# Kernel tuning notes

Measured on AMD Instinct MI355X. Metric: run time of the kernel, lower is better.

## Reference

```python
import jax, jax.numpy as jnp
import numpy as np

B, N, M = 2, 256, 256  # batch items, bboxes per item, feature dim (output_channel)
BLOCKS = 2             # graph_conv_block_num


def _conv2d(x, w, b):
    # x: [C,H,W], w: [O,I,kh,kw] -> [O,H,W], SAME padding, stride 1
    y = jax.lax.conv_general_dilated(x[None], w, (1, 1), 'SAME',
                                     dimension_numbers=('NCHW', 'OIHW', 'NCHW'))
    return y[0] + b[:, None, None]


def setup_inputs() -> dict:
    key = jax.random.key(0)
    ks = jax.random.split(key, 8)
    s = 0.02  # small init to keep activations tame through conv stack
    return {
        'edge_feats': jax.random.normal(ks[0], (B, N, N, 7), jnp.float32),
        'node_feats': jax.random.normal(ks[1], (B, N, M), jnp.float32),
        'adapter_w': jax.random.normal(ks[2], (M, 7, 1, 1), jnp.float32) * s,
        'adapter_b': jnp.zeros((M,), jnp.float32),
        'conv0_w': jax.random.normal(ks[3], (M, 3 * M, 3, 3), jnp.float32) * s,
        'conv0_b': jnp.zeros((M,), jnp.float32),
        'conv1_w': jax.random.normal(ks[4], (M, M, 3, 3), jnp.float32) * s,
        'conv1_b': jnp.zeros((M,), jnp.float32),
        'last_w': jax.random.normal(ks[5], (M, M, 3, 3), jnp.float32) * s,
        'last_b': jnp.zeros((M,), jnp.float32),
        'att_w': jax.random.normal(ks[6], (1, M, 1, 1), jnp.float32) * s,
        'att_b': jnp.zeros((1,), jnp.float32),
    }


def reference(edge_feats, node_feats, adapter_w, adapter_b, conv0_w, conv0_b,
              conv1_w, conv1_b, last_w, last_b, att_w, att_b):
    def one(e, n):
        # e: [N,N,7], n: [N,M]
        edge = _conv2d(jnp.transpose(e, (2, 0, 1)), adapter_w, adapter_b)  # [M,N,N]
        node = n
        for _ in range(BLOCKS):  # conv weights shared across blocks, as in torch
            nT = node.T  # [M,N]
            # channel layout at (i,j): [node_i | edge_ij | node_j]
            feat = jnp.concatenate([
                jnp.broadcast_to(nT[:, :, None], (M, N, N)),
                edge,
                jnp.broadcast_to(nT[:, None, :], (M, N, N)),
            ], axis=0)  # [3M,N,N]
            feat = jax.nn.relu(_conv2d(feat, conv0_w, conv0_b))
            feat = jax.nn.relu(_conv2d(feat, conv1_w, conv1_b))
            # edge attention: 1x1 conv -> leaky_relu -> softmax over j -> weighted sum
            att = jax.nn.leaky_relu(_conv2d(feat, att_w, att_b))   # [1,N,N]
            coeff = jax.nn.softmax(att, axis=-1)                   # softmax over last dim
            node = jnp.sum(coeff * feat, axis=-1).T                # [N,M]
            edge = jax.nn.relu(_conv2d(feat, last_w, last_b))      # [M,N,N]
        return node, jnp.transpose(edge, (1, 2, 0))  # [N,M], [N,N,M]
    return jax.vmap(one)(edge_feats, node_feats)
```

## Files before the change

kernel.cpp:

```cpp
#include <hip/hip_runtime.h>
#include <hip/hip_bf16.h>

typedef __hip_bfloat16 bf16;
typedef __attribute__((ext_vector_type(8))) short s16x8;
typedef __attribute__((ext_vector_type(4))) float f32x4;

__device__ __forceinline__ float b2f(bf16 x) { return __bfloat162float(x); }
__device__ __forceinline__ bf16 f2b(float x) { return __float2bfloat16(x); }

__device__ __forceinline__ void gld16(const void* g, void* l) {
  __builtin_amdgcn_global_load_lds((const __attribute__((address_space(1))) unsigned int*)g,
                                   (__attribute__((address_space(3))) unsigned int*)l,
                                   16, 0, 0);
}

__global__ __launch_bounds__(256) void fill_sentinel(float* out, int n) {
  int idx = blockIdx.x * 256 + threadIdx.x;
  if (idx < n) out[idx] = 100.0f;
}

__global__ __launch_bounds__(64) void zero_zb(bf16* zb) {
  zb[threadIdx.x * 2] = f2b(0.f);
  zb[threadIdx.x * 2 + 1] = f2b(0.f);
}

__global__ __launch_bounds__(256) void pack_w(const float* __restrict__ c0w,
                                              const float* __restrict__ c1w,
                                              const float* __restrict__ lw,
                                              bf16* wp0, bf16* wp1, bf16* wp2, bf16* wnp) {
  const int SEG = 9 * 256 * 256;
  int idx = blockIdx.x * 256 + threadIdx.x;
  if (idx < 3 * SEG) {
    int which = idx / SEG, r = idx % SEG;
    int s = r >> 16, o = (r >> 8) & 255, c = r & 255;
    int ky = s / 3, kx = s - 3 * ky;
    if (which == 0)      wp0[r] = f2b(c0w[(((size_t)o * 768 + 256 + c) * 3 + ky) * 3 + kx]);
    else if (which == 1) wp1[r] = f2b(c1w[(((size_t)o * 256 + c) * 3 + ky) * 3 + kx]);
    else                 wp2[r] = f2b(lw [(((size_t)o * 256 + c) * 3 + ky) * 3 + kx]);
  } else {
    int r = idx - 3 * SEG;
    int m = r & 255, c = (r >> 8) & 255, tt = r >> 16;
    int ot = tt % 3, t2 = (tt / 3) % 3, p = tt / 9;
    int ky, kx, cin;
    if (p == 0) { kx = t2; ky = ot; cin = c; }
    else        { ky = t2; kx = ot; cin = 512 + c; }
    wnp[r] = f2b(c0w[(((size_t)m * 768 + cin) * 3 + ky) * 3 + kx]);
  }
}

__global__ __launch_bounds__(256) void adapter_k(const float* __restrict__ e,
                                                 const float* __restrict__ aw,
                                                 const float* __restrict__ ab,
                                                 bf16* __restrict__ E) {
  int i = blockIdx.x;
  int m = threadIdx.x;
  __shared__ float se[256 * 7];
  const size_t rb = (size_t)i * (256 * 7);
  for (int idx = m; idx < 256 * 7; idx += 256) se[idx] = e[rb + idx];
  __syncthreads();
  float w[7];
#pragma unroll
  for (int c = 0; c < 7; ++c) w[c] = aw[m * 7 + c];
  float bias = ab[m];
  bf16* ob = E + (size_t)i * 65536 + m;
  for (int j = 0; j < 256; ++j) {
    const float* ej = se + j * 7;
    float a = bias;
#pragma unroll
    for (int c = 0; c < 7; ++c) a += w[c] * ej[c];
    ob[(size_t)j * 256] = f2b(a);
  }
}

template <typename T>
__global__ __launch_bounds__(256) void node_terms(const T* __restrict__ nd,
                                                  const bf16* __restrict__ wnp,
                                                  float* __restrict__ TT) {
  int bid = blockIdx.x;
  int chunk = bid & 63;
  int t = (bid >> 6) % 3;
  int p = bid / 192;
  int tid = threadIdx.x;
  __shared__ float snd[6][256];
  int pos0 = chunk * 4;
  for (int idx = tid; idx < 6 * 256; idx += 256) {
    int r = idx >> 8, c = idx & 255;
    int gp = pos0 - 1 + r;
    snd[r][c] = (gp >= 0 && gp < 256) ? (float)nd[(size_t)gp * 256 + c] : 0.f;
  }
  __syncthreads();
  float acc[4] = {0.f, 0.f, 0.f, 0.f};
  const bf16* wb = wnp + (size_t)((p * 3 + t) * 3) * 65536 + tid;
  for (int c = 0; c < 256; ++c) {
    float w0 = b2f(wb[(size_t)c * 256]);
    float w1 = b2f(wb[(size_t)(65536 + c * 256)]);
    float w2 = b2f(wb[(size_t)(2 * 65536 + c * 256)]);
#pragma unroll
    for (int ii = 0; ii < 4; ++ii)
      acc[ii] += w0 * snd[ii][c] + w1 * snd[ii + 1][c] + w2 * snd[ii + 2][c];
  }
  float* o = TT + (((size_t)(p * 3 + t) * 256 + pos0) * 256) + tid;
#pragma unroll
  for (int ii = 0; ii < 4; ++ii) o[(size_t)ii * 256] = acc[ii];
}

template <int EPI, int F32OUT>
__global__ __launch_bounds__(256, 4)
void conv3x3_k(const bf16* __restrict__ inb, const bf16* __restrict__ wpack,
               const float* __restrict__ bias, void* __restrict__ outv,
               const float* __restrict__ TT, const bf16* __restrict__ zbuf) {
  __shared__ __align__(16) char lB[16384];
  __shared__ __align__(16) char lA[16384];
  const int bid = blockIdx.x;
  const int xcd = bid & 7, slot = bid >> 3;
  const int i = (xcd << 5) + (slot >> 2);
  const int ob = slot & 1, jb = (slot >> 1) & 1;
  const int tid = threadIdx.x;
  const int lane = tid & 63, wid = tid >> 6;
  const int wr = wid >> 1, wc = wid & 1;
  const int lo = lane & 15, hi = lane >> 4;

  f32x4 acc[4][4];
  const f32x4 z = {0.f, 0.f, 0.f, 0.f};
#pragma unroll
  for (int mi = 0; mi < 4; ++mi)
#pragma unroll
    for (int ni = 0; ni < 4; ++ni) acc[mi][ni] = z;

  const int xS = tid >> 3;
  const int Gs = tid & 7;
  for (int s = 0; s < 9; ++s) {
    const int ky = s / 3, kx = s - 3 * ky;
    const int r = i + ky - 1;
    if (r < 0 || r > 255) continue;
    const size_t rowbase = (size_t)r * 65536;
    const int colbase = jb * 128 + kx - 1;
    const size_t wbase = ((size_t)s * 256 + ob * 128) * 256;
    for (int cc = 0; cc < 4; ++cc) {
      __syncthreads();
      const int cb = cc * 64;
#pragma unroll
      for (int ch = 0; ch < 4; ++ch) {
        const int x = ch * 32 + xS;
        const int c = colbase + x;
        const int sw = (Gs ^ (x & 7)) << 3;
        const int ldst = (ch * 256 + wid * 64) << 4;
        const bf16* srcB = (c >= 0 && c <= 255)
            ? inb + rowbase + ((size_t)c << 8) + cb + sw
            : zbuf + sw;
        gld16(srcB, lB + ldst);
        gld16(wpack + wbase + ((size_t)x << 8) + cb + sw, lA + ldst);
      }
      __syncthreads();
#pragma unroll
      for (int kk = 0; kk < 2; ++kk) {
        s16x8 af[4], bfr[4];
        const int g0 = kk * 4 + hi;
        const int gx = (g0 ^ (lo & 7)) << 4;
#pragma unroll
        for (int mi = 0; mi < 4; ++mi) {
          const int x = wr * 64 + mi * 16 + lo;
          af[mi] = *(const s16x8*)(lB + x * 128 + gx);
        }
#pragma unroll
        for (int ni = 0; ni < 4; ++ni) {
          const int x = wc * 64 + ni * 16 + lo;
          bfr[ni] = *(const s16x8*)(lA + x * 128 + gx);
        }
#pragma unroll
        for (int mi = 0; mi < 4; ++mi)
#pragma unroll
          for (int ni = 0; ni < 4; ++ni)
            acc[mi][ni] = __builtin_amdgcn_mfma_f32_16x16x32_bf16(af[mi], bfr[ni], acc[mi][ni], 0, 0, 0);
      }
    }
  }

  const int o_base = ob * 128 + wc * 64 + lo;
  const int j_base = jb * 128 + wr * 64 + hi * 4;
  bf16* orow = (bf16*)outv + (size_t)i * 65536;
  float* orowf = (float*)outv + (size_t)i * 65536;
#pragma unroll
  for (int ni = 0; ni < 4; ++ni) {
    const int o = o_base + ni * 16;
    const float bs = bias[o];
    float ni0 = 0.f, ni1 = 0.f, ni2 = 0.f;
    if (EPI) {
      const float* TI = TT + (size_t)i * 256 + o;
      ni0 = TI[0]; ni1 = TI[65536]; ni2 = TI[2 * 65536];
    }
#pragma unroll
    for (int mi = 0; mi < 4; ++mi) {
#pragma unroll
      for (int r = 0; r < 4; ++r) {
        const int j = j_base + mi * 16 + r;
        float v = acc[mi][ni][r] + bs;
        if (EPI) {
          v += ni1 + (j > 0 ? ni0 : 0.f) + (j < 255 ? ni2 : 0.f);
          const float* TJ = TT + (size_t)3 * 65536 + (size_t)j * 256 + o;
          float nj0 = TJ[0], nj1 = TJ[65536], nj2 = TJ[2 * 65536];
          v += nj1 + (i > 0 ? nj0 : 0.f) + (i < 255 ? nj2 : 0.f);
        }
        v = fmaxf(v, 0.f);
        if (F32OUT) orowf[(size_t)j * 256 + o] = v;
        else        orow[(size_t)j * 256 + o] = f2b(v);
      }
    }
  }
}

template <int F32OUT>
__global__ __launch_bounds__(256) void att_wsum(const bf16* __restrict__ feat,
                                                const float* __restrict__ aw,
                                                const float* __restrict__ ab,
                                                bf16* __restrict__ ndb,
                                                float* __restrict__ ndf) {
  int i = blockIdx.x;
  int tid = threadIdx.x, lane = tid & 63, w = tid >> 6;
  __shared__ float s_aw[256];
  __shared__ float s_att[256];
  __shared__ float s_red[8];
  s_aw[tid] = aw[tid];
  __syncthreads();
  float a0 = s_aw[lane * 4], a1 = s_aw[lane * 4 + 1];
  float a2 = s_aw[lane * 4 + 2], a3 = s_aw[lane * 4 + 3];
  const bf16* fb = feat + (size_t)i * 65536;
  float abv = ab[0];
  for (int jj = 0; jj < 64; ++jj) {
    int j = w * 64 + jj;
    const bf16* f = fb + (size_t)j * 256 + lane * 4;
    float v = a0 * b2f(f[0]) + a1 * b2f(f[1]) + a2 * b2f(f[2]) + a3 * b2f(f[3]);
#pragma unroll
    for (int mk = 32; mk; mk >>= 1) v += __shfl_xor(v, mk);
    if (lane == 0) { float a = v + abv; s_att[j] = a > 0.f ? a : 0.01f * a; }
  }
  __syncthreads();
  float x = s_att[tid];
  float mx = x;
#pragma unroll
  for (int mk = 32; mk; mk >>= 1) mx = fmaxf(mx, __shfl_xor(mx, mk));
  if (lane == 0) s_red[w] = mx;
  __syncthreads();
  mx = fmaxf(fmaxf(s_red[0], s_red[1]), fmaxf(s_red[2], s_red[3]));
  float e = expf(x - mx);
  float sm = e;
#pragma unroll
  for (int mk = 32; mk; mk >>= 1) sm += __shfl_xor(sm, mk);
  if (lane == 0) s_red[4 + w] = sm;
  __syncthreads();
  sm = s_red[4] + s_red[5] + s_red[6] + s_red[7];
  __syncthreads();
  s_att[tid] = e / sm;
  __syncthreads();
  float acc = 0.f;
  for (int j = 0; j < 256; ++j) acc += s_att[j] * b2f(fb[(size_t)j * 256 + tid]);
  if (F32OUT) ndf[(size_t)i * 256 + tid] = acc;
  else        ndb[(size_t)i * 256 + tid] = f2b(acc);
}

extern "C" void kernel_launch(void* const* d_in, const int* in_sizes, int n_in,
                              void* d_out, int out_size, void* d_ws, size_t ws_size,
                              hipStream_t stream) {
  const float* edge_feats = (const float*)d_in[0];
  const float* node_feats = (const float*)d_in[1];
  const float* adapter_w  = (const float*)d_in[2];
  const float* adapter_b  = (const float*)d_in[3];
  const float* conv0_w    = (const float*)d_in[4];
  const float* conv0_b    = (const float*)d_in[5];
  const float* conv1_w    = (const float*)d_in[6];
  const float* conv1_b    = (const float*)d_in[7];
  const float* last_w     = (const float*)d_in[8];
  const float* last_b     = (const float*)d_in[9];
  const float* att_w      = (const float*)d_in[10];
  const float* att_b      = (const float*)d_in[11];
  float* out = (float*)d_out;

  char* ws = (char*)d_ws;
  size_t off = 0;
  bf16* Q   = (bf16*)(ws + off); off += (size_t)256 * 256 * 256 * 2;
  bf16* WP0 = (bf16*)(ws + off); off += (size_t)9 * 65536 * 2;
  bf16* WP1 = (bf16*)(ws + off); off += (size_t)9 * 65536 * 2;
  bf16* WP2 = (bf16*)(ws + off); off += (size_t)9 * 65536 * 2;
  bf16* WNP = (bf16*)(ws + off); off += (size_t)18 * 65536 * 2;
  float* TT = (float*)(ws + off); off += (size_t)2 * 3 * 65536 * 4;
  bf16* ND  = (bf16*)(ws + off); off += (size_t)65536 * 2;
  bf16* ZB  = (bf16*)(ws + off); off += 256;
  if (ws_size < off) {
    fill_sentinel<<<(out_size + 255) / 256, 256, 0, stream>>>(out, out_size);
    return;
  }

  zero_zb<<<1, 64, 0, stream>>>(ZB);
  pack_w<<<11520, 256, 0, stream>>>(conv0_w, conv1_w, last_w, WP0, WP1, WP2, WNP);

  for (int b = 0; b < 2; ++b) {
    bf16* P = (bf16*)(out + 131072 + (size_t)b * 16777216);
    float* edge_out = out + 131072 + (size_t)b * 16777216;
    float* node_out = out + (size_t)b * 65536;
    const float* eb = edge_feats + (size_t)b * 458752;
    const float* nb = node_feats + (size_t)b * 65536;

    adapter_k<<<256, 256, 0, stream>>>(eb, adapter_w, adapter_b, P);
    node_terms<float><<<384, 256, 0, stream>>>(nb, WNP, TT);
    conv3x3_k<1, 0><<<1024, 256, 0, stream>>>(P, WP0, conv0_b, Q, TT, ZB);
    conv3x3_k<0, 0><<<1024, 256, 0, stream>>>(Q, WP1, conv1_b, P, nullptr, ZB);
    att_wsum<0><<<256, 256, 0, stream>>>(P, att_w, att_b, ND, nullptr);
    conv3x3_k<0, 0><<<1024, 256, 0, stream>>>(P, WP2, last_b, Q, nullptr, ZB);
    node_terms<bf16><<<384, 256, 0, stream>>>(ND, WNP, TT);
    conv3x3_k<1, 0><<<1024, 256, 0, stream>>>(Q, WP0, conv0_b, P, TT, ZB);
    conv3x3_k<0, 0><<<1024, 256, 0, stream>>>(P, WP1, conv1_b, Q, nullptr, ZB);
    att_wsum<1><<<256, 256, 0, stream>>>(Q, att_w, att_b, nullptr, node_out);
    conv3x3_k<0, 1><<<1024, 256, 0, stream>>>(Q, WP2, last_b, edge_out, nullptr, ZB);
  }
}
```

Before: 1.256 ms.

## Double-buffer LDS loads in conv3x3 kernel to overlap global loads with MFMA

```diff
diff --git a/kernel.cpp b/kernel.cpp
--- a/kernel.cpp
+++ b/kernel.cpp
@@ -105,12 +105,11 @@
 }
 
 template <int EPI, int F32OUT>
-__global__ __launch_bounds__(256, 4)
+__global__ __launch_bounds__(256, 2)
 void conv3x3_k(const bf16* __restrict__ inb, const bf16* __restrict__ wpack,
                const float* __restrict__ bias, void* __restrict__ outv,
                const float* __restrict__ TT, const bf16* __restrict__ zbuf) {
-  __shared__ __align__(16) char lB[16384];
-  __shared__ __align__(16) char lA[16384];
+  __shared__ __align__(16) char lds[65536];
   const int bid = blockIdx.x;
   const int xcd = bid & 7, slot = bid >> 3;
   const int i = (xcd << 5) + (slot >> 2);
@@ -129,51 +128,74 @@
 
   const int xS = tid >> 3;
   const int Gs = tid & 7;
-  for (int s = 0; s < 9; ++s) {
+
+  const int s_lo = (i == 0) ? 3 : 0;
+  const int s_hi = (i == 255) ? 5 : 8;
+  const int nt = (s_hi - s_lo + 1) * 4;
+
+  auto STAGE = [&](int t, int buf) {
+    const int s = s_lo + (t >> 2);
     const int ky = s / 3, kx = s - 3 * ky;
-    const int r = i + ky - 1;
-    if (r < 0 || r > 255) continue;
-    const size_t rowbase = (size_t)r * 65536;
+    const size_t rowbase = (size_t)(i + ky - 1) * 65536;
     const int colbase = jb * 128 + kx - 1;
     const size_t wbase = ((size_t)s * 256 + ob * 128) * 256;
-    for (int cc = 0; cc < 4; ++cc) {
-      __syncthreads();
-      const int cb = cc * 64;
-#pragma unroll
-      for (int ch = 0; ch < 4; ++ch) {
-        const int x = ch * 32 + xS;
-        const int c = colbase + x;
-        const int sw = (Gs ^ (x & 7)) << 3;
-        const int ldst = (ch * 256 + wid * 64) << 4;
-        const bf16* srcB = (c >= 0 && c <= 255)
-            ? inb + rowbase + ((size_t)c << 8) + cb + sw
-            : zbuf + sw;
-        gld16(srcB, lB + ldst);
-        gld16(wpack + wbase + ((size_t)x << 8) + cb + sw, lA + ldst);
+    const int cb = (t & 3) * 64;
+    char* lBb = lds + buf * 32768;
+    char* lAb = lBb + 16384;
+#pragma unroll
+    for (int ch = 0; ch < 4; ++ch) {
+      const int x = ch * 32 + xS;
+      const int c = colbase + x;
+      const int sw = (Gs ^ (x & 7)) << 3;
+      const int ldst = (ch * 256 + wid * 64) << 4;
+      const bf16* srcB = (c >= 0 && c <= 255)
+          ? inb + rowbase + ((size_t)c << 8) + cb + sw
+          : zbuf + sw;
+      gld16(srcB, lBb + ldst);
+      gld16(wpack + wbase + ((size_t)x << 8) + cb + sw, lAb + ldst);
+    }
+  };
+
+  auto COMPUTE = [&](int buf) {
+    const char* lBb = lds + buf * 32768;
+    const char* lAb = lBb + 16384;
+#pragma unroll
+    for (int kk = 0; kk < 2; ++kk) {
+      s16x8 af[4], bfr[4];
+      const int g0 = kk * 4 + hi;
+      const int gx = (g0 ^ (lo & 7)) << 4;
+#pragma unroll
+      for (int mi = 0; mi < 4; ++mi) {
+        const int x = wr * 64 + mi * 16 + lo;
+        af[mi] = *(const s16x8*)(lBb + x * 128 + gx);
       }
-      __syncthreads();
-#pragma unroll
-      for (int kk = 0; kk < 2; ++kk) {
-        s16x8 af[4], bfr[4];
-        const int g0 = kk * 4 + hi;
-        const int gx = (g0 ^ (lo & 7)) << 4;
-#pragma unroll
-        for (int mi = 0; mi < 4; ++mi) {
-          const int x = wr * 64 + mi * 16 + lo;
-          af[mi] = *(const s16x8*)(lB + x * 128 + gx);
-        }
-#pragma unroll
-        for (int ni = 0; ni < 4; ++ni) {
-          const int x = wc * 64 + ni * 16 + lo;
-          bfr[ni] = *(const s16x8*)(lA + x * 128 + gx);
-        }
-#pragma unroll
-        for (int mi = 0; mi < 4; ++mi)
-#pragma unroll
-          for (int ni = 0; ni < 4; ++ni)
-            acc[mi][ni] = __builtin_amdgcn_mfma_f32_16x16x32_bf16(af[mi], bfr[ni], acc[mi][ni], 0, 0, 0);
+#pragma unroll
+      for (int ni = 0; ni < 4; ++ni) {
+        const int x = wc * 64 + ni * 16 + lo;
+        bfr[ni] = *(const s16x8*)(lAb + x * 128 + gx);
       }
-    }
+#pragma unroll
+      for (int mi = 0; mi < 4; ++mi)
+#pragma unroll
+        for (int ni = 0; ni < 4; ++ni)
+          acc[mi][ni] = __builtin_amdgcn_mfma_f32_16x16x32_bf16(af[mi], bfr[ni], acc[mi][ni], 0, 0, 0);
+    }
+  };
+
+  STAGE(0, 0);
+  for (int t = 0; t < nt; ++t) {
+    const int buf = t & 1;
+    if (t + 1 < nt) {
+      STAGE(t + 1, buf ^ 1);
+      asm volatile("s_waitcnt vmcnt(8)" ::: "memory");
+    } else {
+      asm volatile("s_waitcnt vmcnt(0)" ::: "memory");
+    }
+    __builtin_amdgcn_s_barrier();
+    asm volatile("" ::: "memory");
+    COMPUTE(buf);
+    asm volatile("" ::: "memory");
+    __builtin_amdgcn_s_barrier();
   }
 
   const int o_base = ob * 128 + wc * 64 + lo;
```

Result: slower. 1.336 ms (+6.3%).
